# Optimization experiments

Hardware: AMD Instinct MI355X
Metric: run time of the kernel (lower is better)

The kernel has to match this reference:

```python
import jax, jax.numpy as jnp
import numpy as np


def setup_inputs() -> dict:
    key = jax.random.key(0)
    k1, k2 = jax.random.split(key)
    B, H, W, C = 8, 32, 32, 512
    N = 25000
    feature_batch = jax.random.normal(k1, (B, H, W, C), dtype=jnp.float32)
    mb = jax.random.normal(k2, (N, C), dtype=jnp.float32)
    return {"feature_batch": feature_batch, "mb": mb, "b": 9}


def reference(feature_batch, mb, b):
    # feature_batch: (B,H,W,C), mb: (N,C), b: python int
    B, H, W, C = feature_batch.shape
    fv = feature_batch.reshape(B * H * W, C)
    sq_dists = ((fv * fv).sum(1)[:, None]
                + (mb * mb).sum(1)[None, :]
                - 2.0 * fv @ mb.T)                      # (BHW, N)
    pixel_scores = jnp.sqrt(sq_dists.min(axis=1)).reshape(B, H * W)
    # index of most anomalous pixel per image
    idx = jnp.argmax(pixel_scores, axis=1)              # (B,)
    flat_idx = idx + jnp.arange(B) * (H * W)
    selected = fv[flat_idx]                             # (B, C)
    # exact squared distances of selected vectors to full memory bank
    dists_to_mb = ((selected[:, None, :] - mb[None, :, :]) ** 2).sum(-1)  # (B, N)
    # b nearest memory-bank entries (ascending distance order)
    _, b_closest_idx = jax.lax.top_k(-dists_to_mb, b)   # (B, b)
    sel_mb = mb[b_closest_idx]                          # (B, b, C)
    selected_dists = jnp.sqrt(((selected[:, None, :] - sel_mb) ** 2).sum(-1))  # (B, b)
    image_scores = selected_dists[:, 0]
    if b > 1:
        image_scores = image_scores * (1.0 - jax.nn.softmax(selected_dists, axis=1)[:, 0])
    return pixel_scores.reshape(B, 1, H, W), image_scores
```

## Files before the change

### kernel.cpp

```cpp
#include <hip/hip_runtime.h>
#include <hip/hip_bf16.h>

typedef __attribute__((ext_vector_type(8))) short short8;
typedef __attribute__((ext_vector_type(4))) float f32x4;

#define INF_F 3.4e38f

__device__ __forceinline__ void gload16(const void* g, void* l) {
    __builtin_amdgcn_global_load_lds((const __attribute__((address_space(1))) unsigned*)g,
                                     (__attribute__((address_space(3))) unsigned*)l, 16, 0, 0);
}

__global__ void k_conv(const float* __restrict__ fv, const float* __restrict__ mbp,
                       unsigned short* __restrict__ fvb, unsigned short* __restrict__ mbb,
                       float* __restrict__ fnorm, float* __restrict__ mnorm,
                       float* ps_sq, int* ncand, float* cand_val) {
    int t = threadIdx.x, wid = t >> 6, lane = t & 63;
    if (blockIdx.x == 0) {
        if (t == 0) ncand[0] = 0;
        if (t < 64) ((unsigned*)cand_val)[t] = 0x7f800000u;
    }
    int row = blockIdx.x * 4 + wid;
    const float* in; unsigned short* outb; float* norm; int r;
    if (row < 8192) {
        in = fv; outb = fvb; norm = fnorm; r = row;
        if (lane == 0) ((unsigned*)ps_sq)[row] = 0x7f800000u;
    } else if (row < 33192) {
        in = mbp; outb = mbb; norm = mnorm; r = row - 8192;
    } else return;
    const float4* p = (const float4*)(in + (size_t)r * 512) + lane * 2;
    float4 a = p[0], b = p[1];
    float n = a.x*a.x + a.y*a.y + a.z*a.z + a.w*a.w
            + b.x*b.x + b.y*b.y + b.z*b.z + b.w*b.w;
    float vals[8] = {a.x, a.y, a.z, a.w, b.x, b.y, b.z, b.w};
    unsigned short h[8];
    #pragma unroll
    for (int e = 0; e < 8; ++e) {
        unsigned u = __float_as_uint(vals[e]);
        h[e] = (unsigned short)((u + 0x7fffu + ((u >> 16) & 1u)) >> 16);
    }
    *(uint4*)(outb + (size_t)r * 512 + lane * 8) = *(uint4*)h;
    #pragma unroll
    for (int s = 1; s < 64; s <<= 1) n += __shfl_xor(n, s, 64);
    if (lane == 0) norm[r] = n;
}

__global__ __launch_bounds__(256, 2)
void k_gemm_min(const unsigned short* __restrict__ A, const unsigned short* __restrict__ B,
                const float* __restrict__ fnorm, const float* __restrict__ mnorm,
                float* __restrict__ ps_sq) {
    __shared__ unsigned short At[128 * 64];
    __shared__ unsigned short Bt[128 * 64];
    int tid = threadIdx.x, wid = tid >> 6, lane = tid & 63;
    int bid = blockIdx.x;
    int pos = bid >> 3;
    int rb = ((bid & 7) << 3) | (pos & 7);
    int cb = pos >> 3;
    int brow = rb * 128, bcol = cb * 128;
    int wm = (wid >> 1) * 64, wn = (wid & 1) * 64;

    f32x4 acc[4][4] = {};
    int lr = lane >> 3;
    int lkswz = ((lane & 7) ^ lr) * 8;

    for (int k0 = 0; k0 < 512; k0 += 64) {
        #pragma unroll
        for (int c = 0; c < 4; ++c) {
            int ch = wid + c * 4;
            int row = ch * 8 + lr;
            gload16(A + (size_t)(brow + row) * 512 + k0 + lkswz, &At[ch * 512]);
            int srow = bcol + row; if (srow > 24999) srow = 24999;
            gload16(B + (size_t)srow * 512 + k0 + lkswz, &Bt[ch * 512]);
        }
        __syncthreads();
        #pragma unroll
        for (int kk = 0; kk < 2; ++kk) {
            short8 af[4], bf[4];
            int ko = kk * 32 + (lane >> 4) * 8;
            #pragma unroll
            for (int mi = 0; mi < 4; ++mi) {
                int r = wm + mi * 16 + (lane & 15);
                af[mi] = *(const short8*)&At[r * 64 + (ko ^ ((r & 7) << 3))];
            }
            #pragma unroll
            for (int ni = 0; ni < 4; ++ni) {
                int r = wn + ni * 16 + (lane & 15);
                bf[ni] = *(const short8*)&Bt[r * 64 + (ko ^ ((r & 7) << 3))];
            }
            #pragma unroll
            for (int mi = 0; mi < 4; ++mi)
                #pragma unroll
                for (int ni = 0; ni < 4; ++ni)
                    acc[mi][ni] = __builtin_amdgcn_mfma_f32_16x16x32_bf16(af[mi], bf[ni], acc[mi][ni], 0, 0, 0);
        }
        __syncthreads();
    }

    float mnv[4];
    #pragma unroll
    for (int ni = 0; ni < 4; ++ni) {
        int col = bcol + wn + ni * 16 + (lane & 15);
        mnv[ni] = (col < 25000) ? mnorm[col] : INF_F;
    }
    #pragma unroll
    for (int mi = 0; mi < 4; ++mi) {
        #pragma unroll
        for (int r = 0; r < 4; ++r) {
            float v = INF_F;
            #pragma unroll
            for (int ni = 0; ni < 4; ++ni) v = fminf(v, mnv[ni] - 2.0f * acc[mi][ni][r]);
            #pragma unroll
            for (int s = 1; s < 16; s <<= 1) v = fminf(v, __shfl_xor(v, s, 64));
            if ((lane & 15) == 0) {
                int row = brow + wm + mi * 16 + (lane >> 4) * 4 + r;
                float sq = v + fnorm[row];
                atomicMin((unsigned*)&ps_sq[row], __float_as_uint(sq));
            }
        }
    }
}

__global__ void k_cand(const float* __restrict__ ps_sq, float* __restrict__ out0,
                       int* ncand, int* cand_pix, int* cand_batch) {
    __shared__ float smax[4];
    __shared__ int scnt;
    int b = blockIdx.x, t = threadIdx.x, wid = t >> 6, lane = t & 63;
    const float* base = ps_sq + b * 1024;
    float v[4]; float m = -INF_F;
    #pragma unroll
    for (int i = 0; i < 4; ++i) {
        v[i] = base[t + i * 256];
        out0[b * 1024 + t + i * 256] = sqrtf(fmaxf(v[i], 0.0f));
        m = fmaxf(m, v[i]);
    }
    #pragma unroll
    for (int s = 1; s < 64; s <<= 1) m = fmaxf(m, __shfl_xor(m, s, 64));
    if (lane == 0) smax[wid] = m;
    if (t == 0) scnt = 0;
    __syncthreads();
    float bm = fmaxf(fmaxf(smax[0], smax[1]), fmaxf(smax[2], smax[3]));
    #pragma unroll
    for (int i = 0; i < 4; ++i) {
        if (v[i] >= bm - 8.0f) {
            int s = atomicAdd(&scnt, 1);
            if (s < 8) {
                int g = atomicAdd(ncand, 1);
                if (g < 64) { cand_pix[g] = b * 1024 + t + i * 256; cand_batch[g] = b; }
            }
        }
    }
}

__global__ __launch_bounds__(256, 4)
void k_score(const float* __restrict__ fv, const float* __restrict__ mb,
             const int* __restrict__ ncand, const int* __restrict__ cand_pix,
             float* __restrict__ cand_val) {
    int nct = ncand[0]; if (nct > 64) nct = 64;
    int c0 = blockIdx.y * 4;
    if (c0 >= nct) return;
    int t = threadIdx.x, wid = t >> 6, lane = t & 63;

    int p0i = cand_pix[c0];
    int p1i = cand_pix[c0 + 1 < nct ? c0 + 1 : c0];
    int p2i = cand_pix[c0 + 2 < nct ? c0 + 2 : c0];
    int p3i = cand_pix[c0 + 3 < nct ? c0 + 3 : c0];
    const float4* s0 = (const float4*)(fv + (size_t)p0i * 512) + lane * 2;
    const float4* s1 = (const float4*)(fv + (size_t)p1i * 512) + lane * 2;
    const float4* s2 = (const float4*)(fv + (size_t)p2i * 512) + lane * 2;
    const float4* s3 = (const float4*)(fv + (size_t)p3i * 512) + lane * 2;
    float4 ca0 = s0[0], ca1 = s0[1];
    float4 cb0 = s1[0], cb1 = s1[1];
    float4 cc0 = s2[0], cc1 = s2[1];
    float4 cd0 = s3[0], cd1 = s3[1];

    float m0v = INF_F, m1v = INF_F, m2v = INF_F, m3v = INF_F;
    int rbase = blockIdx.x * 64 + wid * 16;
    for (int i = 0; i < 16; ++i) {
        int r = rbase + i;
        if (r >= 25000) break;
        const float4* mp = (const float4*)(mb + (size_t)r * 512) + lane * 2;
        float4 x0 = mp[0], x1 = mp[1];
        float d, p0 = 0.f, p1 = 0.f, p2 = 0.f, p3 = 0.f;
        d = x0.x-ca0.x; p0 += d*d;  d = x0.y-ca0.y; p0 += d*d;  d = x0.z-ca0.z; p0 += d*d;  d = x0.w-ca0.w; p0 += d*d;
        d = x1.x-ca1.x; p0 += d*d;  d = x1.y-ca1.y; p0 += d*d;  d = x1.z-ca1.z; p0 += d*d;  d = x1.w-ca1.w; p0 += d*d;
        d = x0.x-cb0.x; p1 += d*d;  d = x0.y-cb0.y; p1 += d*d;  d = x0.z-cb0.z; p1 += d*d;  d = x0.w-cb0.w; p1 += d*d;
        d = x1.x-cb1.x; p1 += d*d;  d = x1.y-cb1.y; p1 += d*d;  d = x1.z-cb1.z; p1 += d*d;  d = x1.w-cb1.w; p1 += d*d;
        d = x0.x-cc0.x; p2 += d*d;  d = x0.y-cc0.y; p2 += d*d;  d = x0.z-cc0.z; p2 += d*d;  d = x0.w-cc0.w; p2 += d*d;
        d = x1.x-cc1.x; p2 += d*d;  d = x1.y-cc1.y; p2 += d*d;  d = x1.z-cc1.z; p2 += d*d;  d = x1.w-cc1.w; p2 += d*d;
        d = x0.x-cd0.x; p3 += d*d;  d = x0.y-cd0.y; p3 += d*d;  d = x0.z-cd0.z; p3 += d*d;  d = x0.w-cd0.w; p3 += d*d;
        d = x1.x-cd1.x; p3 += d*d;  d = x1.y-cd1.y; p3 += d*d;  d = x1.z-cd1.z; p3 += d*d;  d = x1.w-cd1.w; p3 += d*d;
        #pragma unroll
        for (int s = 1; s < 64; s <<= 1) {
            p0 += __shfl_xor(p0, s, 64);
            p1 += __shfl_xor(p1, s, 64);
            p2 += __shfl_xor(p2, s, 64);
            p3 += __shfl_xor(p3, s, 64);
        }
        m0v = fminf(m0v, p0); m1v = fminf(m1v, p1);
        m2v = fminf(m2v, p2); m3v = fminf(m3v, p3);
    }
    if (lane < 4 && c0 + lane < nct) {
        float mv = (lane == 0) ? m0v : (lane == 1) ? m1v : (lane == 2) ? m2v : m3v;
        atomicMin((unsigned*)&cand_val[c0 + lane], __float_as_uint(mv));
    }
}

__global__ __launch_bounds__(256, 4)
void k_dists4(const float* __restrict__ fv, const float* __restrict__ mb,
              const int* __restrict__ ncand, const int* __restrict__ cand_pix,
              const int* __restrict__ cand_batch, const float* __restrict__ cand_val,
              float* __restrict__ exact_d) {
    int bg = blockIdx.y * 4;
    int t = threadIdx.x, wid = t >> 6, lane = t & 63;
    int n = ncand[0]; if (n > 64) n = 64;

    int sp[4];
    #pragma unroll
    for (int q = 0; q < 4; ++q) {
        float v = -INF_F; int pix = 0x7fffffff;
        if (lane < n && cand_batch[lane] == bg + q) { v = cand_val[lane]; pix = cand_pix[lane]; }
        #pragma unroll
        for (int s = 1; s < 64; s <<= 1) {
            float ov = __shfl_xor(v, s, 64); int oi = __shfl_xor(pix, s, 64);
            if (ov > v || (ov == v && oi < pix)) { v = ov; pix = oi; }
        }
        sp[q] = (pix == 0x7fffffff) ? (bg + q) * 1024 : pix;
    }

    const float4* s0 = (const float4*)(fv + (size_t)sp[0] * 512) + lane * 2;
    const float4* s1 = (const float4*)(fv + (size_t)sp[1] * 512) + lane * 2;
    const float4* s2 = (const float4*)(fv + (size_t)sp[2] * 512) + lane * 2;
    const float4* s3 = (const float4*)(fv + (size_t)sp[3] * 512) + lane * 2;
    float4 ca0 = s0[0], ca1 = s0[1];
    float4 cb0 = s1[0], cb1 = s1[1];
    float4 cc0 = s2[0], cc1 = s2[1];
    float4 cd0 = s3[0], cd1 = s3[1];

    int rbase = blockIdx.x * 64 + wid * 16;
    for (int i = 0; i < 16; ++i) {
        int r = rbase + i;
        if (r >= 25000) break;
        const float4* mp = (const float4*)(mb + (size_t)r * 512) + lane * 2;
        float4 x0 = mp[0], x1 = mp[1];
        float d, p0 = 0.f, p1 = 0.f, p2 = 0.f, p3 = 0.f;
        d = x0.x-ca0.x; p0 += d*d;  d = x0.y-ca0.y; p0 += d*d;  d = x0.z-ca0.z; p0 += d*d;  d = x0.w-ca0.w; p0 += d*d;
        d = x1.x-ca1.x; p0 += d*d;  d = x1.y-ca1.y; p0 += d*d;  d = x1.z-ca1.z; p0 += d*d;  d = x1.w-ca1.w; p0 += d*d;
        d = x0.x-cb0.x; p1 += d*d;  d = x0.y-cb0.y; p1 += d*d;  d = x0.z-cb0.z; p1 += d*d;  d = x0.w-cb0.w; p1 += d*d;
        d = x1.x-cb1.x; p1 += d*d;  d = x1.y-cb1.y; p1 += d*d;  d = x1.z-cb1.z; p1 += d*d;  d = x1.w-cb1.w; p1 += d*d;
        d = x0.x-cc0.x; p2 += d*d;  d = x0.y-cc0.y; p2 += d*d;  d = x0.z-cc0.z; p2 += d*d;  d = x0.w-cc0.w; p2 += d*d;
        d = x1.x-cc1.x; p2 += d*d;  d = x1.y-cc1.y; p2 += d*d;  d = x1.z-cc1.z; p2 += d*d;  d = x1.w-cc1.w; p2 += d*d;
        d = x0.x-cd0.x; p3 += d*d;  d = x0.y-cd0.y; p3 += d*d;  d = x0.z-cd0.z; p3 += d*d;  d = x0.w-cd0.w; p3 += d*d;
        d = x1.x-cd1.x; p3 += d*d;  d = x1.y-cd1.y; p3 += d*d;  d = x1.z-cd1.z; p3 += d*d;  d = x1.w-cd1.w; p3 += d*d;
        #pragma unroll
        for (int s = 1; s < 64; s <<= 1) {
            p0 += __shfl_xor(p0, s, 64);
            p1 += __shfl_xor(p1, s, 64);
            p2 += __shfl_xor(p2, s, 64);
            p3 += __shfl_xor(p3, s, 64);
        }
        if (lane < 4) {
            float pv = (lane == 0) ? p0 : (lane == 1) ? p1 : (lane == 2) ? p2 : p3;
            exact_d[(size_t)(bg + lane) * 25000 + r] = pv;
        }
    }
}

__global__ __launch_bounds__(1024)
void k_final(const float* __restrict__ exact_d, const int* __restrict__ bptr,
             float* __restrict__ out_img) {
    __shared__ float wbv[16]; __shared__ int wbi[16];
    __shared__ float seld[128];
    __shared__ float gbv_s; __shared__ int gbi_s;
    int b = blockIdx.x, t = threadIdx.x, wid = t >> 6, lane = t & 63;
    int bval = bptr[0]; if (bval > 128) bval = 128; if (bval < 1) bval = 1;
    const float* dv = exact_d + (size_t)b * 25000;

    if (bval <= 16) {
        float tv[16]; int ti[16];
        #pragma unroll
        for (int k = 0; k < 16; ++k) { tv[k] = INF_F; ti[k] = 0x7fffffff; }
        for (int r = t; r < 25000; r += 1024) {
            float cv = dv[r]; int ci = r;
            #pragma unroll
            for (int k = 0; k < 16; ++k) {
                bool better = (cv < tv[k]) || (cv == tv[k] && ci < ti[k]);
                if (better) {
                    float t1 = tv[k]; tv[k] = cv; cv = t1;
                    int   t2 = ti[k]; ti[k] = ci; ci = t2;
                }
            }
        }
        for (int k = 0; k < bval; ++k) {
            float bv = tv[0]; int bi = ti[0];
            #pragma unroll
            for (int s = 1; s < 64; s <<= 1) {
                float ov = __shfl_xor(bv, s, 64); int oi = __shfl_xor(bi, s, 64);
                if (ov < bv || (ov == bv && oi < bi)) { bv = ov; bi = oi; }
            }
            if (lane == 0) { wbv[wid] = bv; wbi[wid] = bi; }
            __syncthreads();
            if (t == 0) {
                float fb = wbv[0]; int fi = wbi[0];
                for (int w2 = 1; w2 < 16; ++w2)
                    if (wbv[w2] < fb || (wbv[w2] == fb && wbi[w2] < fi)) { fb = wbv[w2]; fi = wbi[w2]; }
                seld[k] = sqrtf(fb);
                gbv_s = fb; gbi_s = fi;
            }
            __syncthreads();
            if (tv[0] == gbv_s && ti[0] == gbi_s) {
                #pragma unroll
                for (int k2 = 0; k2 < 15; ++k2) { tv[k2] = tv[k2 + 1]; ti[k2] = ti[k2 + 1]; }
                tv[15] = INF_F; ti[15] = 0x7fffffff;
            }
        }
    } else {
        float lastV = -INF_F; int lastI = -1;
        for (int k = 0; k < bval; ++k) {
            float bv = INF_F; int bi = 0x7fffffff;
            for (int r = t; r < 25000; r += 1024) {
                float vv = dv[r];
                bool after = (vv > lastV) || (vv == lastV && r > lastI);
                if (after && (vv < bv || (vv == bv && r < bi))) { bv = vv; bi = r; }
            }
            #pragma unroll
            for (int s = 1; s < 64; s <<= 1) {
                float ov = __shfl_xor(bv, s, 64); int oi = __shfl_xor(bi, s, 64);
                if (ov < bv || (ov == bv && oi < bi)) { bv = ov; bi = oi; }
            }
            if (lane == 0) { wbv[wid] = bv; wbi[wid] = bi; }
            __syncthreads();
            if (t == 0) {
                float fb = wbv[0]; int fi = wbi[0];
                for (int w2 = 1; w2 < 16; ++w2)
                    if (wbv[w2] < fb || (wbv[w2] == fb && wbi[w2] < fi)) { fb = wbv[w2]; fi = wbi[w2]; }
                seld[k] = sqrtf(fb);
                gbv_s = fb; gbi_s = fi;
            }
            __syncthreads();
            lastV = gbv_s; lastI = gbi_s;
        }
    }

    if (t == 0) {
        float d0 = seld[0];
        float img = d0;
        if (bval > 1) {
            float m = -INF_F;
            for (int k = 0; k < bval; ++k) m = fmaxf(m, seld[k]);
            float s = 0.f;
            for (int k = 0; k < bval; ++k) s += expf(seld[k] - m);
            float p0 = expf(seld[0] - m) / s;
            img = d0 * (1.0f - p0);
        }
        out_img[b] = img;
    }
}

extern "C" void kernel_launch(void* const* d_in, const int* in_sizes, int n_in,
                              void* d_out, int out_size, void* d_ws, size_t ws_size,
                              hipStream_t stream) {
    const float* fv = (const float*)d_in[0];
    const float* mb = (const float*)d_in[1];
    const int*   bp = (const int*)d_in[2];
    float* out = (float*)d_out;

    char* w = (char*)d_ws;
    unsigned short* fvb = (unsigned short*)w;
    unsigned short* mbb = (unsigned short*)(w + 8388608);
    size_t o = 8388608 + 25600000;
    float* fnorm    = (float*)(w + o); o += 32768;
    float* mnorm    = (float*)(w + o); o += 100352;
    float* ps_sq    = (float*)(w + o); o += 32768;
    int*   ncand    = (int*)(w + o);   o += 256;
    int*   cand_pix = (int*)(w + o);   o += 256;
    int*   cand_bat = (int*)(w + o);   o += 256;
    float* cand_val = (float*)(w + o); o += 256;
    int*   sel_unused = (int*)(w + o); o += 256;
    float* exact_d  = (float*)(w + o); o += 800000;
    (void)sel_unused;

    k_conv<<<8298, 256, 0, stream>>>(fv, mb, fvb, mbb, fnorm, mnorm, ps_sq, ncand, cand_val);
    k_gemm_min<<<12544, 256, 0, stream>>>(fvb, mbb, fnorm, mnorm, ps_sq);
    k_cand<<<8, 256, 0, stream>>>(ps_sq, out, ncand, cand_pix, cand_bat);
    k_score<<<dim3(391, 16), 256, 0, stream>>>(fv, mb, ncand, cand_pix, cand_val);
    k_dists4<<<dim3(391, 2), 256, 0, stream>>>(fv, mb, ncand, cand_pix, cand_bat, cand_val, exact_d);
    k_final<<<8, 1024, 0, stream>>>(exact_d, bp, out + 8192);
}
```

Before: 480.5 us.

## Fuse tail kernels into one cooperative kernel with grid syncs

Merges the candidate selection, candidate scoring, exact distance and top-k/final kernels into a single cooperative launch of 1024 blocks separated by grid-wide syncs, cutting three kernel launch gaps. Scoring work is distributed over a grid-stride loop instead of a 2D grid, and the final top-k stage now runs with 256 threads per block instead of 1024. If the cooperative launch fails, it falls back to four separate launches with a mode argument. Grid syncs and the smaller final block add their own cost.

```diff
diff --git a/kernel.cpp b/kernel.cpp
--- a/kernel.cpp
+++ b/kernel.cpp
@@ -1,5 +1,8 @@
 #include <hip/hip_runtime.h>
 #include <hip/hip_bf16.h>
+#include <hip/hip_cooperative_groups.h>
+
+namespace cg = cooperative_groups;
 
 typedef __attribute__((ext_vector_type(8))) short short8;
 typedef __attribute__((ext_vector_type(4))) float f32x4;
@@ -120,239 +123,241 @@
     }
 }
 
-__global__ void k_cand(const float* __restrict__ ps_sq, float* __restrict__ out0,
-                       int* ncand, int* cand_pix, int* cand_batch) {
-    __shared__ float smax[4];
-    __shared__ int scnt;
-    int b = blockIdx.x, t = threadIdx.x, wid = t >> 6, lane = t & 63;
-    const float* base = ps_sq + b * 1024;
-    float v[4]; float m = -INF_F;
-    #pragma unroll
-    for (int i = 0; i < 4; ++i) {
-        v[i] = base[t + i * 256];
-        out0[b * 1024 + t + i * 256] = sqrtf(fmaxf(v[i], 0.0f));
-        m = fmaxf(m, v[i]);
-    }
-    #pragma unroll
-    for (int s = 1; s < 64; s <<= 1) m = fmaxf(m, __shfl_xor(m, s, 64));
-    if (lane == 0) smax[wid] = m;
-    if (t == 0) scnt = 0;
-    __syncthreads();
-    float bm = fmaxf(fmaxf(smax[0], smax[1]), fmaxf(smax[2], smax[3]));
-    #pragma unroll
-    for (int i = 0; i < 4; ++i) {
-        if (v[i] >= bm - 8.0f) {
-            int s = atomicAdd(&scnt, 1);
-            if (s < 8) {
-                int g = atomicAdd(ncand, 1);
-                if (g < 64) { cand_pix[g] = b * 1024 + t + i * 256; cand_batch[g] = b; }
-            }
-        }
-    }
-}
-
 __global__ __launch_bounds__(256, 4)
-void k_score(const float* __restrict__ fv, const float* __restrict__ mb,
-             const int* __restrict__ ncand, const int* __restrict__ cand_pix,
-             float* __restrict__ cand_val) {
-    int nct = ncand[0]; if (nct > 64) nct = 64;
-    int c0 = blockIdx.y * 4;
-    if (c0 >= nct) return;
+void k_tail(const float* __restrict__ fv, const float* __restrict__ mb,
+            const float* __restrict__ ps_sq, float* __restrict__ out0,
+            int* ncand, int* cand_pix, int* cand_bat, float* cand_val,
+            float* __restrict__ exact_d, const int* __restrict__ bp,
+            float* __restrict__ out_img, int mode) {
+    cg::grid_group grid = cg::this_grid();
+    __shared__ float s_smax[4]; __shared__ int s_scnt;
+    __shared__ float s_wbv[4]; __shared__ int s_wbi[4];
+    __shared__ float s_seld[128];
+    __shared__ float s_gbv; __shared__ int s_gbi;
+
     int t = threadIdx.x, wid = t >> 6, lane = t & 63;
 
-    int p0i = cand_pix[c0];
-    int p1i = cand_pix[c0 + 1 < nct ? c0 + 1 : c0];
-    int p2i = cand_pix[c0 + 2 < nct ? c0 + 2 : c0];
-    int p3i = cand_pix[c0 + 3 < nct ? c0 + 3 : c0];
-    const float4* s0 = (const float4*)(fv + (size_t)p0i * 512) + lane * 2;
-    const float4* s1 = (const float4*)(fv + (size_t)p1i * 512) + lane * 2;
-    const float4* s2 = (const float4*)(fv + (size_t)p2i * 512) + lane * 2;
-    const float4* s3 = (const float4*)(fv + (size_t)p3i * 512) + lane * 2;
-    float4 ca0 = s0[0], ca1 = s0[1];
-    float4 cb0 = s1[0], cb1 = s1[1];
-    float4 cc0 = s2[0], cc1 = s2[1];
-    float4 cd0 = s3[0], cd1 = s3[1];
-
-    float m0v = INF_F, m1v = INF_F, m2v = INF_F, m3v = INF_F;
-    int rbase = blockIdx.x * 64 + wid * 16;
-    for (int i = 0; i < 16; ++i) {
-        int r = rbase + i;
-        if (r >= 25000) break;
-        const float4* mp = (const float4*)(mb + (size_t)r * 512) + lane * 2;
-        float4 x0 = mp[0], x1 = mp[1];
-        float d, p0 = 0.f, p1 = 0.f, p2 = 0.f, p3 = 0.f;
-        d = x0.x-ca0.x; p0 += d*d;  d = x0.y-ca0.y; p0 += d*d;  d = x0.z-ca0.z; p0 += d*d;  d = x0.w-ca0.w; p0 += d*d;
-        d = x1.x-ca1.x; p0 += d*d;  d = x1.y-ca1.y; p0 += d*d;  d = x1.z-ca1.z; p0 += d*d;  d = x1.w-ca1.w; p0 += d*d;
-        d = x0.x-cb0.x; p1 += d*d;  d = x0.y-cb0.y; p1 += d*d;  d = x0.z-cb0.z; p1 += d*d;  d = x0.w-cb0.w; p1 += d*d;
-        d = x1.x-cb1.x; p1 += d*d;  d = x1.y-cb1.y; p1 += d*d;  d = x1.z-cb1.z; p1 += d*d;  d = x1.w-cb1.w; p1 += d*d;
-        d = x0.x-cc0.x; p2 += d*d;  d = x0.y-cc0.y; p2 += d*d;  d = x0.z-cc0.z; p2 += d*d;  d = x0.w-cc0.w; p2 += d*d;
-        d = x1.x-cc1.x; p2 += d*d;  d = x1.y-cc1.y; p2 += d*d;  d = x1.z-cc1.z; p2 += d*d;  d = x1.w-cc1.w; p2 += d*d;
-        d = x0.x-cd0.x; p3 += d*d;  d = x0.y-cd0.y; p3 += d*d;  d = x0.z-cd0.z; p3 += d*d;  d = x0.w-cd0.w; p3 += d*d;
-        d = x1.x-cd1.x; p3 += d*d;  d = x1.y-cd1.y; p3 += d*d;  d = x1.z-cd1.z; p3 += d*d;  d = x1.w-cd1.w; p3 += d*d;
-        #pragma unroll
-        for (int s = 1; s < 64; s <<= 1) {
-            p0 += __shfl_xor(p0, s, 64);
-            p1 += __shfl_xor(p1, s, 64);
-            p2 += __shfl_xor(p2, s, 64);
-            p3 += __shfl_xor(p3, s, 64);
-        }
-        m0v = fminf(m0v, p0); m1v = fminf(m1v, p1);
-        m2v = fminf(m2v, p2); m3v = fminf(m3v, p3);
-    }
-    if (lane < 4 && c0 + lane < nct) {
-        float mv = (lane == 0) ? m0v : (lane == 1) ? m1v : (lane == 2) ? m2v : m3v;
-        atomicMin((unsigned*)&cand_val[c0 + lane], __float_as_uint(mv));
-    }
-}
-
-__global__ __launch_bounds__(256, 4)
-void k_dists4(const float* __restrict__ fv, const float* __restrict__ mb,
-              const int* __restrict__ ncand, const int* __restrict__ cand_pix,
-              const int* __restrict__ cand_batch, const float* __restrict__ cand_val,
-              float* __restrict__ exact_d) {
-    int bg = blockIdx.y * 4;
-    int t = threadIdx.x, wid = t >> 6, lane = t & 63;
-    int n = ncand[0]; if (n > 64) n = 64;
-
-    int sp[4];
-    #pragma unroll
-    for (int q = 0; q < 4; ++q) {
-        float v = -INF_F; int pix = 0x7fffffff;
-        if (lane < n && cand_batch[lane] == bg + q) { v = cand_val[lane]; pix = cand_pix[lane]; }
-        #pragma unroll
-        for (int s = 1; s < 64; s <<= 1) {
-            float ov = __shfl_xor(v, s, 64); int oi = __shfl_xor(pix, s, 64);
-            if (ov > v || (ov == v && oi < pix)) { v = ov; pix = oi; }
-        }
-        sp[q] = (pix == 0x7fffffff) ? (bg + q) * 1024 : pix;
-    }
-
-    const float4* s0 = (const float4*)(fv + (size_t)sp[0] * 512) + lane * 2;
-    const float4* s1 = (const float4*)(fv + (size_t)sp[1] * 512) + lane * 2;
-    const float4* s2 = (const float4*)(fv + (size_t)sp[2] * 512) + lane * 2;
-    const float4* s3 = (const float4*)(fv + (size_t)sp[3] * 512) + lane * 2;
-    float4 ca0 = s0[0], ca1 = s0[1];
-    float4 cb0 = s1[0], cb1 = s1[1];
-    float4 cc0 = s2[0], cc1 = s2[1];
-    float4 cd0 = s3[0], cd1 = s3[1];
-
-    int rbase = blockIdx.x * 64 + wid * 16;
-    for (int i = 0; i < 16; ++i) {
-        int r = rbase + i;
-        if (r >= 25000) break;
-        const float4* mp = (const float4*)(mb + (size_t)r * 512) + lane * 2;
-        float4 x0 = mp[0], x1 = mp[1];
-        float d, p0 = 0.f, p1 = 0.f, p2 = 0.f, p3 = 0.f;
-        d = x0.x-ca0.x; p0 += d*d;  d = x0.y-ca0.y; p0 += d*d;  d = x0.z-ca0.z; p0 += d*d;  d = x0.w-ca0.w; p0 += d*d;
-        d = x1.x-ca1.x; p0 += d*d;  d = x1.y-ca1.y; p0 += d*d;  d = x1.z-ca1.z; p0 += d*d;  d = x1.w-ca1.w; p0 += d*d;
-        d = x0.x-cb0.x; p1 += d*d;  d = x0.y-cb0.y; p1 += d*d;  d = x0.z-cb0.z; p1 += d*d;  d = x0.w-cb0.w; p1 += d*d;
-        d = x1.x-cb1.x; p1 += d*d;  d = x1.y-cb1.y; p1 += d*d;  d = x1.z-cb1.z; p1 += d*d;  d = x1.w-cb1.w; p1 += d*d;
-        d = x0.x-cc0.x; p2 += d*d;  d = x0.y-cc0.y; p2 += d*d;  d = x0.z-cc0.z; p2 += d*d;  d = x0.w-cc0.w; p2 += d*d;
-        d = x1.x-cc1.x; p2 += d*d;  d = x1.y-cc1.y; p2 += d*d;  d = x1.z-cc1.z; p2 += d*d;  d = x1.w-cc1.w; p2 += d*d;
-        d = x0.x-cd0.x; p3 += d*d;  d = x0.y-cd0.y; p3 += d*d;  d = x0.z-cd0.z; p3 += d*d;  d = x0.w-cd0.w; p3 += d*d;
-        d = x1.x-cd1.x; p3 += d*d;  d = x1.y-cd1.y; p3 += d*d;  d = x1.z-cd1.z; p3 += d*d;  d = x1.w-cd1.w; p3 += d*d;
-        #pragma unroll
-        for (int s = 1; s < 64; s <<= 1) {
-            p0 += __shfl_xor(p0, s, 64);
-            p1 += __shfl_xor(p1, s, 64);
-            p2 += __shfl_xor(p2, s, 64);
-            p3 += __shfl_xor(p3, s, 64);
-        }
-        if (lane < 4) {
-            float pv = (lane == 0) ? p0 : (lane == 1) ? p1 : (lane == 2) ? p2 : p3;
-            exact_d[(size_t)(bg + lane) * 25000 + r] = pv;
-        }
-    }
-}
-
-__global__ __launch_bounds__(1024)
-void k_final(const float* __restrict__ exact_d, const int* __restrict__ bptr,
-             float* __restrict__ out_img) {
-    __shared__ float wbv[16]; __shared__ int wbi[16];
-    __shared__ float seld[128];
-    __shared__ float gbv_s; __shared__ int gbi_s;
-    int b = blockIdx.x, t = threadIdx.x, wid = t >> 6, lane = t & 63;
-    int bval = bptr[0]; if (bval > 128) bval = 128; if (bval < 1) bval = 1;
-    const float* dv = exact_d + (size_t)b * 25000;
-
-    if (bval <= 16) {
-        float tv[16]; int ti[16];
-        #pragma unroll
-        for (int k = 0; k < 16; ++k) { tv[k] = INF_F; ti[k] = 0x7fffffff; }
-        for (int r = t; r < 25000; r += 1024) {
-            float cv = dv[r]; int ci = r;
-            #pragma unroll
-            for (int k = 0; k < 16; ++k) {
-                bool better = (cv < tv[k]) || (cv == tv[k] && ci < ti[k]);
-                if (better) {
-                    float t1 = tv[k]; tv[k] = cv; cv = t1;
-                    int   t2 = ti[k]; ti[k] = ci; ci = t2;
-                }
-            }
-        }
-        for (int k = 0; k < bval; ++k) {
-            float bv = tv[0]; int bi = ti[0];
-            #pragma unroll
-            for (int s = 1; s < 64; s <<= 1) {
-                float ov = __shfl_xor(bv, s, 64); int oi = __shfl_xor(bi, s, 64);
-                if (ov < bv || (ov == bv && oi < bi)) { bv = ov; bi = oi; }
-            }
-            if (lane == 0) { wbv[wid] = bv; wbi[wid] = bi; }
+    if (mode < 0 || mode == 0) {
+        if (blockIdx.x < 8) {
+            int b = blockIdx.x;
+            const float* base = ps_sq + b * 1024;
+            float v[4]; float m = -INF_F;
+            #pragma unroll
+            for (int i = 0; i < 4; ++i) {
+                v[i] = base[t + i * 256];
+                out0[b * 1024 + t + i * 256] = sqrtf(fmaxf(v[i], 0.0f));
+                m = fmaxf(m, v[i]);
+            }
+            #pragma unroll
+            for (int s = 1; s < 64; s <<= 1) m = fmaxf(m, __shfl_xor(m, s, 64));
+            if (lane == 0) s_smax[wid] = m;
+            if (t == 0) s_scnt = 0;
             __syncthreads();
+            float bm = fmaxf(fmaxf(s_smax[0], s_smax[1]), fmaxf(s_smax[2], s_smax[3]));
+            #pragma unroll
+            for (int i = 0; i < 4; ++i) {
+                if (v[i] >= bm - 8.0f) {
+                    int s = atomicAdd(&s_scnt, 1);
+                    if (s < 8) {
+                        int g = atomicAdd(ncand, 1);
+                        if (g < 64) { cand_pix[g] = b * 1024 + t + i * 256; cand_bat[g] = b; }
+                    }
+                }
+            }
+        }
+    }
+    if (mode < 0) { __threadfence(); grid.sync(); }
+
+    if (mode < 0 || mode == 1) {
+        int nct = ncand[0]; if (nct > 64) nct = 64;
+        int nitems = ((nct + 3) >> 2) * 391;
+        for (int item = blockIdx.x; item < nitems; item += gridDim.x) {
+            int c0 = (item / 391) * 4;
+            int chunk = item % 391;
+            int p0i = cand_pix[c0];
+            int p1i = cand_pix[c0 + 1 < nct ? c0 + 1 : c0];
+            int p2i = cand_pix[c0 + 2 < nct ? c0 + 2 : c0];
+            int p3i = cand_pix[c0 + 3 < nct ? c0 + 3 : c0];
+            const float4* s0 = (const float4*)(fv + (size_t)p0i * 512) + lane * 2;
+            const float4* s1 = (const float4*)(fv + (size_t)p1i * 512) + lane * 2;
+            const float4* s2 = (const float4*)(fv + (size_t)p2i * 512) + lane * 2;
+            const float4* s3 = (const float4*)(fv + (size_t)p3i * 512) + lane * 2;
+            float4 ca0 = s0[0], ca1 = s0[1];
+            float4 cb0 = s1[0], cb1 = s1[1];
+            float4 cc0 = s2[0], cc1 = s2[1];
+            float4 cd0 = s3[0], cd1 = s3[1];
+            float m0v = INF_F, m1v = INF_F, m2v = INF_F, m3v = INF_F;
+            int rbase = chunk * 64 + wid * 16;
+            for (int i = 0; i < 16; ++i) {
+                int r = rbase + i;
+                if (r >= 25000) break;
+                const float4* mp = (const float4*)(mb + (size_t)r * 512) + lane * 2;
+                float4 x0 = mp[0], x1 = mp[1];
+                float d, p0 = 0.f, p1 = 0.f, p2 = 0.f, p3 = 0.f;
+                d = x0.x-ca0.x; p0 += d*d;  d = x0.y-ca0.y; p0 += d*d;  d = x0.z-ca0.z; p0 += d*d;  d = x0.w-ca0.w; p0 += d*d;
+                d = x1.x-ca1.x; p0 += d*d;  d = x1.y-ca1.y; p0 += d*d;  d = x1.z-ca1.z; p0 += d*d;  d = x1.w-ca1.w; p0 += d*d;
+                d = x0.x-cb0.x; p1 += d*d;  d = x0.y-cb0.y; p1 += d*d;  d = x0.z-cb0.z; p1 += d*d;  d = x0.w-cb0.w; p1 += d*d;
+                d = x1.x-cb1.x; p1 += d*d;  d = x1.y-cb1.y; p1 += d*d;  d = x1.z-cb1.z; p1 += d*d;  d = x1.w-cb1.w; p1 += d*d;
+                d = x0.x-cc0.x; p2 += d*d;  d = x0.y-cc0.y; p2 += d*d;  d = x0.z-cc0.z; p2 += d*d;  d = x0.w-cc0.w; p2 += d*d;
+                d = x1.x-cc1.x; p2 += d*d;  d = x1.y-cc1.y; p2 += d*d;  d = x1.z-cc1.z; p2 += d*d;  d = x1.w-cc1.w; p2 += d*d;
+                d = x0.x-cd0.x; p3 += d*d;  d = x0.y-cd0.y; p3 += d*d;  d = x0.z-cd0.z; p3 += d*d;  d = x0.w-cd0.w; p3 += d*d;
+                d = x1.x-cd1.x; p3 += d*d;  d = x1.y-cd1.y; p3 += d*d;  d = x1.z-cd1.z; p3 += d*d;  d = x1.w-cd1.w; p3 += d*d;
+                #pragma unroll
+                for (int s = 1; s < 64; s <<= 1) {
+                    p0 += __shfl_xor(p0, s, 64);
+                    p1 += __shfl_xor(p1, s, 64);
+                    p2 += __shfl_xor(p2, s, 64);
+                    p3 += __shfl_xor(p3, s, 64);
+                }
+                m0v = fminf(m0v, p0); m1v = fminf(m1v, p1);
+                m2v = fminf(m2v, p2); m3v = fminf(m3v, p3);
+            }
+            if (lane < 4 && c0 + lane < nct) {
+                float mv = (lane == 0) ? m0v : (lane == 1) ? m1v : (lane == 2) ? m2v : m3v;
+                atomicMin((unsigned*)&cand_val[c0 + lane], __float_as_uint(mv));
+            }
+        }
+    }
+    if (mode < 0) { __threadfence(); grid.sync(); }
+
+    if (mode < 0 || mode == 2) {
+        if (blockIdx.x < 782) {
+            int item = blockIdx.x;
+            int bg = (item / 391) * 4;
+            int chunk = item % 391;
+            int n = ncand[0]; if (n > 64) n = 64;
+            int sp0, sp1, sp2, sp3;
+#define WINNER(Q, OUTV) do { float v = -INF_F; int pix = 0x7fffffff; \
+            if (lane < n && cand_bat[lane] == bg + (Q)) { v = cand_val[lane]; pix = cand_pix[lane]; } \
+            for (int s = 1; s < 64; s <<= 1) { \
+                float ov = __shfl_xor(v, s, 64); int oi = __shfl_xor(pix, s, 64); \
+                if (ov > v || (ov == v && oi < pix)) { v = ov; pix = oi; } } \
+            OUTV = (pix == 0x7fffffff) ? (bg + (Q)) * 1024 : pix; } while (0)
+            WINNER(0, sp0); WINNER(1, sp1); WINNER(2, sp2); WINNER(3, sp3);
+#undef WINNER
+            const float4* s0 = (const float4*)(fv + (size_t)sp0 * 512) + lane * 2;
+            const float4* s1 = (const float4*)(fv + (size_t)sp1 * 512) + lane * 2;
+            const float4* s2 = (const float4*)(fv + (size_t)sp2 * 512) + lane * 2;
+            const float4* s3 = (const float4*)(fv + (size_t)sp3 * 512) + lane * 2;
+            float4 ca0 = s0[0], ca1 = s0[1];
+            float4 cb0 = s1[0], cb1 = s1[1];
+            float4 cc0 = s2[0], cc1 = s2[1];
+            float4 cd0 = s3[0], cd1 = s3[1];
+            int rbase = chunk * 64 + wid * 16;
+            for (int i = 0; i < 16; ++i) {
+                int r = rbase + i;
+                if (r >= 25000) break;
+                const float4* mp = (const float4*)(mb + (size_t)r * 512) + lane * 2;
+                float4 x0 = mp[0], x1 = mp[1];
+                float d, p0 = 0.f, p1 = 0.f, p2 = 0.f, p3 = 0.f;
+                d = x0.x-ca0.x; p0 += d*d;  d = x0.y-ca0.y; p0 += d*d;  d = x0.z-ca0.z; p0 += d*d;  d = x0.w-ca0.w; p0 += d*d;
+                d = x1.x-ca1.x; p0 += d*d;  d = x1.y-ca1.y; p0 += d*d;  d = x1.z-ca1.z; p0 += d*d;  d = x1.w-ca1.w; p0 += d*d;
+                d = x0.x-cb0.x; p1 += d*d;  d = x0.y-cb0.y; p1 += d*d;  d = x0.z-cb0.z; p1 += d*d;  d = x0.w-cb0.w; p1 += d*d;
+                d = x1.x-cb1.x; p1 += d*d;  d = x1.y-cb1.y; p1 += d*d;  d = x1.z-cb1.z; p1 += d*d;  d = x1.w-cb1.w; p1 += d*d;
+                d = x0.x-cc0.x; p2 += d*d;  d = x0.y-cc0.y; p2 += d*d;  d = x0.z-cc0.z; p2 += d*d;  d = x0.w-cc0.w; p2 += d*d;
+                d = x1.x-cc1.x; p2 += d*d;  d = x1.y-cc1.y; p2 += d*d;  d = x1.z-cc1.z; p2 += d*d;  d = x1.w-cc1.w; p2 += d*d;
+                d = x0.x-cd0.x; p3 += d*d;  d = x0.y-cd0.y; p3 += d*d;  d = x0.z-cd0.z; p3 += d*d;  d = x0.w-cd0.w; p3 += d*d;
+                d = x1.x-cd1.x; p3 += d*d;  d = x1.y-cd1.y; p3 += d*d;  d = x1.z-cd1.z; p3 += d*d;  d = x1.w-cd1.w; p3 += d*d;
+                #pragma unroll
+                for (int s = 1; s < 64; s <<= 1) {
+                    p0 += __shfl_xor(p0, s, 64);
+                    p1 += __shfl_xor(p1, s, 64);
+                    p2 += __shfl_xor(p2, s, 64);
+                    p3 += __shfl_xor(p3, s, 64);
+                }
+                if (lane < 4) {
+                    float pv = (lane == 0) ? p0 : (lane == 1) ? p1 : (lane == 2) ? p2 : p3;
+                    exact_d[(size_t)(bg + lane) * 25000 + r] = pv;
+                }
+            }
+        }
+    }
+    if (mode < 0) { __threadfence(); grid.sync(); }
+
+    if (mode < 0 || mode == 3) {
+        if (blockIdx.x < 8) {
+            int b = blockIdx.x;
+            int bval = bp[0]; if (bval > 128) bval = 128; if (bval < 1) bval = 1;
+            const float* dv = exact_d + (size_t)b * 25000;
+            if (bval <= 16) {
+                float tv[16]; int ti[16];
+                #pragma unroll
+                for (int k = 0; k < 16; ++k) { tv[k] = INF_F; ti[k] = 0x7fffffff; }
+                for (int r = t; r < 25000; r += 256) {
+                    float cv = dv[r]; int ci = r;
+                    #pragma unroll
+                    for (int k = 0; k < 16; ++k) {
+                        bool better = (cv < tv[k]) || (cv == tv[k] && ci < ti[k]);
+                        if (better) {
+                            float t1 = tv[k]; tv[k] = cv; cv = t1;
+                            int   t2 = ti[k]; ti[k] = ci; ci = t2;
+                        }
+                    }
+                }
+                for (int k = 0; k < bval; ++k) {
+                    float bv = tv[0]; int bi = ti[0];
+                    #pragma unroll
+                    for (int s = 1; s < 64; s <<= 1) {
+                        float ov = __shfl_xor(bv, s, 64); int oi = __shfl_xor(bi, s, 64);
+                        if (ov < bv || (ov == bv && oi < bi)) { bv = ov; bi = oi; }
+                    }
+                    if (lane == 0) { s_wbv[wid] = bv; s_wbi[wid] = bi; }
+                    __syncthreads();
+                    if (t == 0) {
+                        float fb = s_wbv[0]; int fi = s_wbi[0];
+                        for (int w2 = 1; w2 < 4; ++w2)
+                            if (s_wbv[w2] < fb || (s_wbv[w2] == fb && s_wbi[w2] < fi)) { fb = s_wbv[w2]; fi = s_wbi[w2]; }
+                        s_seld[k] = sqrtf(fb);
+                        s_gbv = fb; s_gbi = fi;
+                    }
+                    __syncthreads();
+                    if (tv[0] == s_gbv && ti[0] == s_gbi) {
+                        #pragma unroll
+                        for (int k2 = 0; k2 < 15; ++k2) { tv[k2] = tv[k2 + 1]; ti[k2] = ti[k2 + 1]; }
+                        tv[15] = INF_F; ti[15] = 0x7fffffff;
+                    }
+                }
+            } else {
+                float lastV = -INF_F; int lastI = -1;
+                for (int k = 0; k < bval; ++k) {
+                    float bv = INF_F; int bi = 0x7fffffff;
+                    for (int r = t; r < 25000; r += 256) {
+                        float vv = dv[r];
+                        bool after = (vv > lastV) || (vv == lastV && r > lastI);
+                        if (after && (vv < bv || (vv == bv && r < bi))) { bv = vv; bi = r; }
+                    }
+                    #pragma unroll
+                    for (int s = 1; s < 64; s <<= 1) {
+                        float ov = __shfl_xor(bv, s, 64); int oi = __shfl_xor(bi, s, 64);
+                        if (ov < bv || (ov == bv && oi < bi)) { bv = ov; bi = oi; }
+                    }
+                    if (lane == 0) { s_wbv[wid] = bv; s_wbi[wid] = bi; }
+                    __syncthreads();
+                    if (t == 0) {
+                        float fb = s_wbv[0]; int fi = s_wbi[0];
+                        for (int w2 = 1; w2 < 4; ++w2)
+                            if (s_wbv[w2] < fb || (s_wbv[w2] == fb && s_wbi[w2] < fi)) { fb = s_wbv[w2]; fi = s_wbi[w2]; }
+                        s_seld[k] = sqrtf(fb);
+                        s_gbv = fb; s_gbi = fi;
+                    }
+                    __syncthreads();
+                    lastV = s_gbv; lastI = s_gbi;
+                }
+            }
             if (t == 0) {
-                float fb = wbv[0]; int fi = wbi[0];
-                for (int w2 = 1; w2 < 16; ++w2)
-                    if (wbv[w2] < fb || (wbv[w2] == fb && wbi[w2] < fi)) { fb = wbv[w2]; fi = wbi[w2]; }
-                seld[k] = sqrtf(fb);
-                gbv_s = fb; gbi_s = fi;
-            }
-            __syncthreads();
-            if (tv[0] == gbv_s && ti[0] == gbi_s) {
-                #pragma unroll
-                for (int k2 = 0; k2 < 15; ++k2) { tv[k2] = tv[k2 + 1]; ti[k2] = ti[k2 + 1]; }
-                tv[15] = INF_F; ti[15] = 0x7fffffff;
-            }
-        }
-    } else {
-        float lastV = -INF_F; int lastI = -1;
-        for (int k = 0; k < bval; ++k) {
-            float bv = INF_F; int bi = 0x7fffffff;
-            for (int r = t; r < 25000; r += 1024) {
-                float vv = dv[r];
-                bool after = (vv > lastV) || (vv == lastV && r > lastI);
-                if (after && (vv < bv || (vv == bv && r < bi))) { bv = vv; bi = r; }
-            }
-            #pragma unroll
-            for (int s = 1; s < 64; s <<= 1) {
-                float ov = __shfl_xor(bv, s, 64); int oi = __shfl_xor(bi, s, 64);
-                if (ov < bv || (ov == bv && oi < bi)) { bv = ov; bi = oi; }
-            }
-            if (lane == 0) { wbv[wid] = bv; wbi[wid] = bi; }
-            __syncthreads();
-            if (t == 0) {
-                float fb = wbv[0]; int fi = wbi[0];
-                for (int w2 = 1; w2 < 16; ++w2)
-                    if (wbv[w2] < fb || (wbv[w2] == fb && wbi[w2] < fi)) { fb = wbv[w2]; fi = wbi[w2]; }
-                seld[k] = sqrtf(fb);
-                gbv_s = fb; gbi_s = fi;
-            }
-            __syncthreads();
-            lastV = gbv_s; lastI = gbi_s;
-        }
-    }
-
-    if (t == 0) {
-        float d0 = seld[0];
-        float img = d0;
-        if (bval > 1) {
-            float m = -INF_F;
-            for (int k = 0; k < bval; ++k) m = fmaxf(m, seld[k]);
-            float s = 0.f;
-            for (int k = 0; k < bval; ++k) s += expf(seld[k] - m);
-            float p0 = expf(seld[0] - m) / s;
-            img = d0 * (1.0f - p0);
-        }
-        out_img[b] = img;
+                float d0 = s_seld[0];
+                float img = d0;
+                if (bval > 1) {
+                    float m = -INF_F;
+                    for (int k = 0; k < bval; ++k) m = fmaxf(m, s_seld[k]);
+                    float s = 0.f;
+                    for (int k = 0; k < bval; ++k) s += expf(s_seld[k] - m);
+                    float p0 = expf(s_seld[0] - m) / s;
+                    img = d0 * (1.0f - p0);
+                }
+                out_img[b] = img;
+            }
+        }
     }
 }
 
@@ -381,8 +386,21 @@
 
     k_conv<<<8298, 256, 0, stream>>>(fv, mb, fvb, mbb, fnorm, mnorm, ps_sq, ncand, cand_val);
     k_gemm_min<<<12544, 256, 0, stream>>>(fvb, mbb, fnorm, mnorm, ps_sq);
-    k_cand<<<8, 256, 0, stream>>>(ps_sq, out, ncand, cand_pix, cand_bat);
-    k_score<<<dim3(391, 16), 256, 0, stream>>>(fv, mb, ncand, cand_pix, cand_val);
-    k_dists4<<<dim3(391, 2), 256, 0, stream>>>(fv, mb, ncand, cand_pix, cand_bat, cand_val, exact_d);
-    k_final<<<8, 1024, 0, stream>>>(exact_d, bp, out + 8192);
+
+    float* out0 = out;
+    float* oimg = out + 8192;
+    int mode = -1;
+    const float* fv_a = fv; const float* mb_a = mb; const float* ps_a = ps_sq;
+    const int* bp_a = bp;
+    void* args[] = { (void*)&fv_a, (void*)&mb_a, (void*)&ps_a, (void*)&out0,
+                     (void*)&ncand, (void*)&cand_pix, (void*)&cand_bat, (void*)&cand_val,
+                     (void*)&exact_d, (void*)&bp_a, (void*)&oimg, (void*)&mode };
+    hipError_t e = hipLaunchCooperativeKernel((const void*)k_tail, dim3(1024), dim3(256),
+                                              args, 0, stream);
+    if (e != hipSuccess) {
+        (void)hipGetLastError();
+        for (int m = 0; m < 4; ++m)
+            k_tail<<<1024, 256, 0, stream>>>(fv, mb, ps_sq, out0, ncand, cand_pix, cand_bat,
+                                             cand_val, exact_d, bp, oimg, m);
+    }
 }
```

Result: slower. 1.131 ms (+135.3%).
